# Kernel optimization log

Measured on AMD Instinct MI355X. Metric: run time of the kernel, lower is better.

The kernel has to match this reference:

```python
import jax, jax.numpy as jnp
import numpy as np

N, E, B, H, L = 100000, 200000, 2048, 256, 4
EPS_MSG = 1e-7   # GENConv message eps
LN_EPS = 1e-5    # torch LayerNorm default eps
SM_EPS = 1e-16   # PyG softmax denominator eps


def layer_norm(x, g, b):
    mu = x.mean(-1, keepdims=True)
    var = ((x - mu) ** 2).mean(-1, keepdims=True)
    return (x - mu) * jax.lax.rsqrt(var + LN_EPS) * g + b


def gen_conv(x, src, dst, eattr, t, W1, b1, lg, lb, W2, b2):
    # GENConv(aggr='softmax', learn_t, num_layers=2, norm='layer')
    msg = jax.nn.relu(x[src] + eattr) + EPS_MSG                      # [E,H]
    scaled = msg * t
    seg_max = jax.ops.segment_max(scaled, dst, num_segments=N)       # [N,H]
    seg_max = jnp.where(jnp.isfinite(seg_max), seg_max, 0.0)
    ex = jnp.exp(scaled - seg_max[dst])                              # [E,H]
    denom = jax.ops.segment_sum(ex, dst, num_segments=N)             # [N,H]
    alpha = ex / (denom[dst] + SM_EPS)
    out = jax.ops.segment_sum(msg * alpha, dst, num_segments=N)      # [N,H]
    out = out + x                                                    # root residual inside GENConv
    h = jax.nn.relu(layer_norm(out @ W1 + b1, lg, lb))               # MLP: Lin -> LN -> ReLU -> Lin
    return h @ W2 + b2


def setup_inputs() -> dict:
    key = jax.random.key(0)
    ks = iter(jax.random.split(key, 16))
    s = lambda *sh: jax.random.normal(next(ks), sh, jnp.float32) * 0.05
    return dict(
        x=jax.random.normal(next(ks), (N, 9), jnp.float32),
        edge_index=jax.random.randint(next(ks), (2, E), 0, N),
        edge_attr=jax.random.normal(next(ks), (E, 3), jnp.float32),
        batch=jnp.sort(jax.random.randint(next(ks), (N,), 0, B)),
        node_W=s(9, H), node_b=jnp.zeros((H,), jnp.float32),
        edge_W=s(3, H), edge_b=jnp.zeros((H,), jnp.float32),
        vn_emb=jnp.zeros((1, H), jnp.float32),
        ln_g=jnp.ones((L, H), jnp.float32), ln_b=jnp.zeros((L, H), jnp.float32),
        t=jnp.ones((L - 1,), jnp.float32),
        mlp_W1=s(L - 1, H, 2 * H), mlp_b1=jnp.zeros((L - 1, 2 * H), jnp.float32),
        mlp_ln_g=jnp.ones((L - 1, 2 * H), jnp.float32), mlp_ln_b=jnp.zeros((L - 1, 2 * H), jnp.float32),
        mlp_W2=s(L - 1, 2 * H, H), mlp_b2=jnp.zeros((L - 1, H), jnp.float32),
    )


def reference(x, edge_index, edge_attr, batch, node_W, node_b, edge_W, edge_b,
              vn_emb, ln_g, ln_b, t, mlp_W1, mlp_b1, mlp_ln_g, mlp_ln_b, mlp_W2, mlp_b2):
    src, dst = edge_index[0], edge_index[1]
    h = x @ node_W + node_b                                          # node encoder
    ea = edge_attr @ edge_W + edge_b                                 # edge encoder
    vn = jnp.broadcast_to(vn_emb, (B, H))
    counts = jax.ops.segment_sum(jnp.ones((N,), h.dtype), batch, num_segments=B)
    inv_counts = (1.0 / jnp.maximum(counts, 1.0))[:, None]           # [B,1]
    # layers[1:] run conv (block='res+'); layers[0] supplies only the final norm+act
    for l in range(1, L):
        hn = jax.nn.relu(layer_norm(h, ln_g[l], ln_b[l]))            # dropout=0.1 is a no-op in eval
        h = h + gen_conv(hn, src, dst, ea, t[l - 1],
                         mlp_W1[l - 1], mlp_b1[l - 1], mlp_ln_g[l - 1], mlp_ln_b[l - 1],
                         mlp_W2[l - 1], mlp_b2[l - 1])
        vn = vn + jax.ops.segment_sum(h, batch, num_segments=B) * inv_counts  # scatter_mean
        h = h + vn[batch]                                            # broadcast virtual node
    h = jax.nn.relu(layer_norm(h, ln_g[0], ln_b[0]))
    return jax.ops.segment_sum(h, batch, num_segments=B) * inv_counts  # global_mean_pool [B,H]
```

## Files before the change

kernel.cpp:

```cpp
#include <hip/hip_runtime.h>
#include <cstdint>
#include <cstddef>


typedef _Float16 half8_t __attribute__((ext_vector_type(8)));
typedef _Float16 half4_t __attribute__((ext_vector_type(4)));
typedef float    floatx4 __attribute__((ext_vector_type(4)));

#define DEVINL __device__ __forceinline__

DEVINL float wave_sum(float v) {
#pragma unroll
  for (int m = 32; m; m >>= 1) v += __shfl_xor(v, m, 64);
  return v;
}

__global__ __launch_bounds__(256) void k_node_enc(
    const float* __restrict__ x, const float* __restrict__ W,
    const float* __restrict__ bias, _Float16* __restrict__ h, int Nr) {
  __shared__ float sW[9 * 256];
  __shared__ float sb[256];
  __shared__ float sx[72];
  const int j = threadIdx.x;
#pragma unroll
  for (int k = 0; k < 9; ++k) sW[k * 256 + j] = W[k * 256 + j];
  sb[j] = bias[j];
  const int row0 = blockIdx.x * 8;
  if (j < 72) {
    int p = row0 * 9 + j;
    sx[j] = (p < Nr * 9) ? x[p] : 0.f;
  }
  __syncthreads();
  for (int r = 0; r < 8; ++r) {
    int row = row0 + r;
    if (row >= Nr) break;
    float acc = sb[j];
#pragma unroll
    for (int k = 0; k < 9; ++k) acc = fmaf(sx[r * 9 + k], sW[k * 256 + j], acc);
    h[(size_t)row * 256 + j] = (_Float16)acc;
  }
}

__global__ void k_bptr(const int* __restrict__ batch, int* __restrict__ bptr,
                       int N_, int B_) {
  int b = blockIdx.x * 256 + threadIdx.x;
  if (b > B_) return;
  int lo = 0, hi = N_;
  while (lo < hi) {
    int mid = (lo + hi) >> 1;
    if (batch[mid] < b) lo = mid + 1; else hi = mid;
  }
  bptr[b] = lo;
}

__global__ void k_deg(const int* __restrict__ ei, int* __restrict__ deg, int E_) {
  int e = blockIdx.x * 256 + threadIdx.x;
  if (e < E_) atomicAdd(&deg[ei[E_ + e]], 1);
}

__global__ __launch_bounds__(256) void k_scan1(
    const int* __restrict__ in, int* __restrict__ out1, int* __restrict__ bsum, int n) {
  __shared__ int tmp[256];
  const int t = threadIdx.x;
  const int base = blockIdx.x * 1024;
  int v[4];
  int run = 0;
#pragma unroll
  for (int i = 0; i < 4; ++i) {
    int p = base + t * 4 + i;
    int xv = (p < n) ? in[p] : 0;
    run += xv;
    v[i] = run;
  }
  tmp[t] = run;
  __syncthreads();
  for (int off = 1; off < 256; off <<= 1) {
    int u = (t >= off) ? tmp[t - off] : 0;
    __syncthreads();
    tmp[t] += u;
    __syncthreads();
  }
  int excl = tmp[t] - run;
#pragma unroll
  for (int i = 0; i < 4; ++i) {
    int p = base + t * 4 + i;
    if (p < n) out1[p] = v[i] + excl;
  }
  if (t == 255) bsum[blockIdx.x] = tmp[255];
}

__global__ void k_scan2(int* bsum, int nb, int* ptr0) {
  if (threadIdx.x == 0 && blockIdx.x == 0) {
    int run = 0;
    for (int i = 0; i < nb; ++i) { int xv = bsum[i]; bsum[i] = run; run += xv; }
    ptr0[0] = 0;
  }
}

__global__ __launch_bounds__(256) void k_scan3(
    int* out1, const int* __restrict__ bsum, int* __restrict__ cursor, int n) {
  int add = bsum[blockIdx.x];
  int p0 = blockIdx.x * 1024 + threadIdx.x * 4;
#pragma unroll
  for (int i = 0; i < 4; ++i) {
    int p = p0 + i;
    if (p < n) {
      int v = out1[p] + add;
      out1[p] = v;
      cursor[p + 1] = v;
    }
  }
  if (blockIdx.x == 0 && threadIdx.x == 0) cursor[0] = 0;
}

__global__ void k_csrfill(const int* __restrict__ ei, int* __restrict__ cursor,
                          int* __restrict__ csr_src, int* __restrict__ csr_eid, int E_) {
  int e = blockIdx.x * 256 + threadIdx.x;
  if (e < E_) {
    int d = ei[E_ + e];
    int pos = atomicAdd(&cursor[d], 1);
    csr_src[pos] = ei[e];
    csr_eid[pos] = e;
  }
}

__global__ void k_vninit(const float* __restrict__ emb, float* __restrict__ vn) {
  vn[(size_t)blockIdx.x * 256 + threadIdx.x] = emb[threadIdx.x];
}

__global__ __launch_bounds__(256) void k_wcvt_all(
    const float* __restrict__ W1, const float* __restrict__ W2,
    _Float16* __restrict__ W1T, _Float16* __restrict__ W2T) {
  int idx = blockIdx.x * 256 + threadIdx.x;
  int mat = idx >> 17;
  int rem = idx & 131071;
  if (mat < 3) {
    int k = rem >> 9, n = rem & 511;
    W1T[(size_t)mat * 131072 + (size_t)n * 256 + k] =
        (_Float16)W1[(size_t)mat * 131072 + rem];
  } else {
    int m = mat - 3;
    int k = rem >> 8, n = rem & 255;
    W2T[(size_t)m * 131072 + (size_t)n * 512 + k] =
        (_Float16)W2[(size_t)m * 131072 + rem];
  }
}

__global__ __launch_bounds__(256) void k_ln256(
    const _Float16* __restrict__ h, const float* __restrict__ g,
    const float* __restrict__ b, _Float16* __restrict__ out, int Nr) {
  int row = blockIdx.x * 4 + (threadIdx.x >> 6);
  if (row >= Nr) return;
  int lane = threadIdx.x & 63;
  half4_t xh = *(const half4_t*)(h + (size_t)row * 256 + lane * 4);
  float x0 = (float)xh[0], x1 = (float)xh[1], x2 = (float)xh[2], x3 = (float)xh[3];
  float s = wave_sum(x0 + x1 + x2 + x3);
  float mu = s * (1.f / 256.f);
  float d0 = x0 - mu, d1 = x1 - mu, d2 = x2 - mu, d3 = x3 - mu;
  float v = wave_sum(d0 * d0 + d1 * d1 + d2 * d2 + d3 * d3);
  float rstd = rsqrtf(v * (1.f / 256.f) + 1e-5f);
  float4 gv = *(const float4*)(g + lane * 4);
  float4 bv = *(const float4*)(b + lane * 4);
  half4_t o;
  o[0] = (_Float16)fmaxf(d0 * rstd * gv.x + bv.x, 0.f);
  o[1] = (_Float16)fmaxf(d1 * rstd * gv.y + bv.y, 0.f);
  o[2] = (_Float16)fmaxf(d2 * rstd * gv.z + bv.z, 0.f);
  o[3] = (_Float16)fmaxf(d3 * rstd * gv.w + bv.w, 0.f);
  *(half4_t*)(out + (size_t)row * 256 + lane * 4) = o;
}

__global__ __launch_bounds__(256) void k_aggregate(
    const _Float16* __restrict__ hn, const float* __restrict__ eattr,
    const float* __restrict__ edgeW, const float* __restrict__ edgeB,
    const int* __restrict__ indptr, const int* __restrict__ csr_src,
    const int* __restrict__ csr_eid, const float* __restrict__ tptr,
    _Float16* __restrict__ agg, int Nr) {
  int node = blockIdx.x * 4 + (threadIdx.x >> 6);
  if (node >= Nr) return;
  int lane = threadIdx.x & 63;
  int j0 = lane * 4;
  float4 w0 = *(const float4*)(edgeW + j0);
  float4 w1 = *(const float4*)(edgeW + 256 + j0);
  float4 w2 = *(const float4*)(edgeW + 512 + j0);
  float4 wb = *(const float4*)(edgeB + j0);
  float W0[4] = {w0.x, w0.y, w0.z, w0.w};
  float W1r[4] = {w1.x, w1.y, w1.z, w1.w};
  float W2r[4] = {w2.x, w2.y, w2.z, w2.w};
  float WB[4] = {wb.x, wb.y, wb.z, wb.w};
  float tval = tptr[0];
  int e0 = indptr[node], e1 = indptr[node + 1];
  float D[4] = {0.f, 0.f, 0.f, 0.f};
  float Nu[4] = {0.f, 0.f, 0.f, 0.f};
  for (int s = e0; s < e1; ++s) {
    int srcn = csr_src[s];
    int eid = csr_eid[s];
    float ex0 = eattr[(size_t)eid * 3 + 0];
    float ex1 = eattr[(size_t)eid * 3 + 1];
    float ex2 = eattr[(size_t)eid * 3 + 2];
    half4_t hv = *(const half4_t*)(hn + (size_t)srcn * 256 + j0);
#pragma unroll
    for (int i = 0; i < 4; ++i) {
      float eaj = fmaf(ex0, W0[i], fmaf(ex1, W1r[i], fmaf(ex2, W2r[i], WB[i])));
      float msg = fmaxf((float)hv[i] + eaj, 0.f) + 1e-7f;
      float pr = __expf(msg * tval);
      D[i] += pr;
      Nu[i] = fmaf(pr, msg, Nu[i]);
    }
  }
  half4_t hs = *(const half4_t*)(hn + (size_t)node * 256 + j0);
  half4_t res;
#pragma unroll
  for (int i = 0; i < 4; ++i)
    res[i] = (_Float16)(Nu[i] / (D[i] + 1e-16f) + (float)hs[i]);
  *(half4_t*)(agg + (size_t)node * 256 + j0) = res;
}

__global__ __launch_bounds__(256, 2) void k_gemm1(
    const _Float16* __restrict__ A, const _Float16* __restrict__ BT,
    const float* __restrict__ bias, _Float16* __restrict__ outh,
    float2* __restrict__ rstat, int M) {
  constexpr int EPS = 132;
  __shared__ _Float16 ldsA[64 * 256];
  __shared__ _Float16 ldsB[128 * 64];
  __shared__ _Float16 ldsE[4 * 16 * EPS];
  const int tid = threadIdx.x;
  const int lane = tid & 63;
  const int wv = tid >> 6;
  const int m0 = blockIdx.x * 64;
  const int wm = wv * 16;
  const int q = lane >> 4;
  const int l16 = lane & 15;
  _Float16* epi = ldsE + wv * (16 * EPS);

  {
    half8_t tmp[8];
    int ss[8];
#pragma unroll
    for (int g = 0; g < 8; ++g) {
      int s = g * 256 + tid;
      int r = s >> 5;
      int c = (s & 31) ^ (r & 7);
      int rowA = m0 + r;
      rowA = rowA < M ? rowA : (M - 1);
      tmp[g] = *(const half8_t*)(A + (size_t)rowA * 256 + c * 8);
      ss[g] = s;
    }
#pragma unroll
    for (int g = 0; g < 8; ++g)
      *(half8_t*)(ldsA + (size_t)ss[g] * 8) = tmp[g];
  }

  size_t offB[4];
  int ldsOffB[4];
#pragma unroll
  for (int i = 0; i < 4; ++i) {
    int p = (i * 4 + wv) * 64 + lane;
    int r = p >> 3;
    int s = p & 7;
    int gg = s ^ (r & 7);
    offB[i] = (size_t)r * 256 + gg * 8;
    ldsOffB[i] = p * 8;
  }
  half8_t rb[4];
  auto loadB = [&](int j) {
    int n = j >> 2, t = j & 3;
    size_t base = (size_t)n * 128 * 256 + t * 64;
#pragma unroll
    for (int i = 0; i < 4; ++i)
      rb[i] = *(const half8_t*)(BT + base + offB[i]);
  };
  auto writeB = [&]() {
#pragma unroll
    for (int i = 0; i < 4; ++i)
      *(half8_t*)(ldsB + ldsOffB[i]) = rb[i];
  };

  floatx4 acc[8] = {};
  float sA[4] = {0.f, 0.f, 0.f, 0.f}, s2A[4] = {0.f, 0.f, 0.f, 0.f};

  loadB(0);
  writeB();
  for (int j = 0; j < 16; ++j) {
    __syncthreads();
    if (j + 1 < 16) loadB(j + 1);
    const int t = j & 3;
#pragma unroll
    for (int kk = 0; kk < 2; ++kk) {
      const int c8 = kk * 4 + q;
      const int cg = t * 8 + c8;
      int r = wm + l16;
      half8_t af = *(const half8_t*)(ldsA + (size_t)(r * 32 + (cg ^ (r & 7))) * 8);
      half8_t bf[8];
#pragma unroll
      for (int ct = 0; ct < 8; ++ct) {
        int n = ct * 16 + l16;
        bf[ct] = *(const half8_t*)(ldsB + (size_t)(n * 8 + (c8 ^ (n & 7))) * 8);
      }
#pragma unroll
      for (int ct = 0; ct < 8; ++ct)
        acc[ct] = __builtin_amdgcn_mfma_f32_16x16x32_f16(af, bf[ct], acc[ct], 0, 0, 0);
    }
    __syncthreads();
    if (j + 1 < 16) writeB();
    if ((j & 3) == 3) {
      int n = j >> 2;
#pragma unroll
      for (int rr = 0; rr < 4; ++rr) {
        int rloc = q * 4 + rr;
        float s = 0.f, s2 = 0.f;
#pragma unroll
        for (int ct = 0; ct < 8; ++ct) {
          int col = n * 128 + ct * 16 + l16;
          float v = acc[ct][rr] + bias[col];
          epi[rloc * EPS + ct * 16 + l16] = (_Float16)v;
          s += v;
          s2 += v * v;
        }
        sA[rr] += s;
        s2A[rr] += s2;
      }
#pragma unroll
      for (int it = 0; it < 4; ++it) {
        int rloc = it * 4 + q;
        int row = m0 + wm + rloc;
        if (row < M) {
          half8_t ev = *(const half8_t*)(epi + rloc * EPS + l16 * 8);
          *(half8_t*)(outh + (size_t)row * 512 + n * 128 + l16 * 8) = ev;
        }
      }
#pragma unroll
      for (int ct = 0; ct < 8; ++ct)
        acc[ct] = floatx4{0.f, 0.f, 0.f, 0.f};
    }
  }

#pragma unroll
  for (int rr = 0; rr < 4; ++rr) {
    float s = sA[rr], s2 = s2A[rr];
#pragma unroll
    for (int m = 1; m < 16; m <<= 1) {
      s += __shfl_xor(s, m, 64);
      s2 += __shfl_xor(s2, m, 64);
    }
    int row = m0 + wm + q * 4 + rr;
    if (l16 == 0 && row < M) rstat[row] = make_float2(s, s2);
  }
}

template <int VN>
__global__ __launch_bounds__(256, 2) void k_gemm2(
    const _Float16* __restrict__ A, const _Float16* __restrict__ BT,
    const float* __restrict__ bias, const float2* __restrict__ rstat,
    const float* __restrict__ lg, const float* __restrict__ lb,
    const float* __restrict__ vn, const int* __restrict__ batch,
    _Float16* __restrict__ outf, int M) {
  constexpr int K = 512, NN = 256, NT = K / 64;
  constexpr int EPS = 68;
  const int g = blockIdx.x;
  const int mI = blockIdx.y * 8 + (g & 7);
  const int nI = g >> 3;
  const int mT = (M + 127) >> 7;
  if (mI >= mT) return;

  __shared__ _Float16 ldsbuf[4 * 64 * EPS];
  _Float16* ldsA = ldsbuf;
  _Float16* ldsB = ldsbuf + 128 * 64;
  __shared__ float sg[512];
  __shared__ float sbt[512];
  const int tid = threadIdx.x;
  sg[tid] = lg[tid];
  sg[tid + 256] = lg[tid + 256];
  sbt[tid] = lb[tid];
  sbt[tid + 256] = lb[tid + 256];
  __syncthreads();

  const int lane = tid & 63;
  const int wv = tid >> 6;
  const int m0 = mI * 128;
  const int n0 = nI * 128;
  const int wm = (wv >> 1) * 64;
  const int wn = (wv & 1) * 64;
  const int q = lane >> 4;
  const int l16 = lane & 15;
  floatx4 acc[4][4] = {};

  size_t offA[4], offB[4];
  int ldsOff[4], gcolA[4];
  float aco[4], cco[4];
#pragma unroll
  for (int i = 0; i < 4; ++i) {
    int p = (i * 4 + wv) * 64 + lane;
    int r = p >> 3;
    int s = p & 7;
    int gg = s ^ (r & 7);
    int rowA = m0 + r;
    rowA = rowA < M ? rowA : (M - 1);
    offA[i] = (size_t)rowA * K + gg * 8;
    offB[i] = (size_t)(n0 + r) * K + gg * 8;
    ldsOff[i] = p * 8;
    gcolA[i] = gg * 8;
    float2 st = rstat[rowA];
    float mu = st.x * (1.f / 512.f);
    float var = st.y * (1.f / 512.f) - mu * mu;
    float rs = rsqrtf(var + 1e-5f);
    aco[i] = rs;
    cco[i] = -mu * rs;
  }
  half8_t ra[4], rb[4];
  auto loadtile = [&](int kt) {
#pragma unroll
    for (int i = 0; i < 4; ++i) {
      ra[i] = *(const half8_t*)(A + offA[i] + kt);
      rb[i] = *(const half8_t*)(BT + offB[i] + kt);
    }
  };
  auto writetile = [&](int kt) {
#pragma unroll
    for (int i = 0; i < 4; ++i) {
      int c0 = kt + gcolA[i];
      half8_t ya;
#pragma unroll
      for (int jj = 0; jj < 8; ++jj) {
        float e = fmaf((float)ra[i][jj], aco[i], cco[i]);
        float y = fmaf(e, sg[c0 + jj], sbt[c0 + jj]);
        ya[jj] = (_Float16)fmaxf(y, 0.f);
      }
      *(half8_t*)(ldsA + ldsOff[i]) = ya;
      *(half8_t*)(ldsB + ldsOff[i]) = rb[i];
    }
  };

  loadtile(0);
  writetile(0);
#pragma unroll
  for (int t = 0; t < NT; ++t) {
    __syncthreads();
    if (t + 1 < NT) loadtile((t + 1) * 64);
#pragma unroll
    for (int kk = 0; kk < 2; ++kk) {
      half8_t af[4], bf[4];
      const int c8 = kk * 4 + q;
#pragma unroll
      for (int rt = 0; rt < 4; ++rt) {
        int r = wm + rt * 16 + l16;
        af[rt] = *(const half8_t*)(ldsA + (size_t)(r * 8 + (c8 ^ (r & 7))) * 8);
      }
#pragma unroll
      for (int ct = 0; ct < 4; ++ct) {
        int n = wn + ct * 16 + l16;
        bf[ct] = *(const half8_t*)(ldsB + (size_t)(n * 8 + (c8 ^ (n & 7))) * 8);
      }
#pragma unroll
      for (int rt = 0; rt < 4; ++rt)
#pragma unroll
        for (int ct = 0; ct < 4; ++ct)
          acc[rt][ct] = __builtin_amdgcn_mfma_f32_16x16x32_f16(af[rt], bf[ct], acc[rt][ct], 0, 0, 0);
    }
    __syncthreads();
    if (t + 1 < NT) writetile((t + 1) * 64);
  }

  _Float16* epi = ldsbuf + wv * (64 * EPS);
#pragma unroll
  for (int rt = 0; rt < 4; ++rt) {
#pragma unroll
    for (int rr = 0; rr < 4; ++rr) {
      int rloc = rt * 16 + q * 4 + rr;
      int row = m0 + wm + rloc;
      int rowc = row < M ? row : (M - 1);
      int bb = 0;
      if constexpr (VN) bb = batch[rowc];
#pragma unroll
      for (int ct = 0; ct < 4; ++ct) {
        int cloc = ct * 16 + l16;
        int col = n0 + wn + cloc;
        float v = acc[rt][ct][rr] + bias[col];
        if constexpr (VN) v += vn[(size_t)bb * 256 + col];
        epi[rloc * EPS + cloc] = (_Float16)v;
      }
    }
  }
#pragma unroll
  for (int it = 0; it < 8; ++it) {
    int rloc = it * 8 + (lane >> 3);
    int row = m0 + wm + rloc;
    if (row < M) {
      int c0 = (lane & 7) * 8;
      size_t gidx = (size_t)row * NN + n0 + wn + c0;
      half8_t hv = *(const half8_t*)(outf + gidx);
      half8_t ev = *(const half8_t*)(epi + rloc * EPS + c0);
      half8_t o;
#pragma unroll
      for (int jj = 0; jj < 8; ++jj) o[jj] = (_Float16)((float)hv[jj] + (float)ev[jj]);
      *(half8_t*)(outf + gidx) = o;
    }
  }
}

__global__ __launch_bounds__(256) void k_vnln(
    const _Float16* __restrict__ h, float* __restrict__ vn,
    const int* __restrict__ bptr, const float* __restrict__ g,
    const float* __restrict__ b, _Float16* __restrict__ hn) {
  __shared__ float red[3][256];
  __shared__ float svn[256];
  int bb = blockIdx.x;
  int w = threadIdx.x >> 6;
  int lane = threadIdx.x & 63;
  int n0 = bptr[bb], n1 = bptr[bb + 1];
  float a0 = 0.f, a1 = 0.f, a2 = 0.f, a3 = 0.f;
  for (int row = n0 + w; row < n1; row += 4) {
    half4_t xh = *(const half4_t*)(h + (size_t)row * 256 + lane * 4);
    a0 += (float)xh[0]; a1 += (float)xh[1];
    a2 += (float)xh[2]; a3 += (float)xh[3];
  }
  if (w > 0) {
    red[w - 1][lane * 4 + 0] = a0;
    red[w - 1][lane * 4 + 1] = a1;
    red[w - 1][lane * 4 + 2] = a2;
    red[w - 1][lane * 4 + 3] = a3;
  }
  __syncthreads();
  if (w == 0) {
    int c = n1 - n0;
    float ic = 1.f / (float)(c > 1 ? c : 1);
#pragma unroll
    for (int k = 0; k < 3; ++k) {
      a0 += red[k][lane * 4 + 0];
      a1 += red[k][lane * 4 + 1];
      a2 += red[k][lane * 4 + 2];
      a3 += red[k][lane * 4 + 3];
    }
    float4 vo = *(const float4*)(vn + (size_t)bb * 256 + lane * 4);
    vo.x += a0 * ic; vo.y += a1 * ic; vo.z += a2 * ic; vo.w += a3 * ic;
    *(float4*)(vn + (size_t)bb * 256 + lane * 4) = vo;
    svn[lane * 4 + 0] = vo.x;
    svn[lane * 4 + 1] = vo.y;
    svn[lane * 4 + 2] = vo.z;
    svn[lane * 4 + 3] = vo.w;
  }
  __syncthreads();
  float4 vv = *(const float4*)(svn + lane * 4);
  float4 gv = *(const float4*)(g + lane * 4);
  float4 bv = *(const float4*)(b + lane * 4);
  for (int row = n0 + w; row < n1; row += 4) {
    half4_t xh = *(const half4_t*)(h + (size_t)row * 256 + lane * 4);
    float x0 = (float)xh[0] + vv.x, x1 = (float)xh[1] + vv.y;
    float x2 = (float)xh[2] + vv.z, x3 = (float)xh[3] + vv.w;
    float s = wave_sum(x0 + x1 + x2 + x3);
    float mu = s * (1.f / 256.f);
    float d0 = x0 - mu, d1 = x1 - mu, d2 = x2 - mu, d3 = x3 - mu;
    float v = wave_sum(d0 * d0 + d1 * d1 + d2 * d2 + d3 * d3);
    float rstd = rsqrtf(v * (1.f / 256.f) + 1e-5f);
    half4_t o;
    o[0] = (_Float16)fmaxf(d0 * rstd * gv.x + bv.x, 0.f);
    o[1] = (_Float16)fmaxf(d1 * rstd * gv.y + bv.y, 0.f);
    o[2] = (_Float16)fmaxf(d2 * rstd * gv.z + bv.z, 0.f);
    o[3] = (_Float16)fmaxf(d3 * rstd * gv.w + bv.w, 0.f);
    *(half4_t*)(hn + (size_t)row * 256 + lane * 4) = o;
  }
}

__global__ __launch_bounds__(256) void k_vnlnpool(
    const _Float16* __restrict__ h, const float* __restrict__ vn,
    const int* __restrict__ bptr, const float* __restrict__ g,
    const float* __restrict__ b, float* __restrict__ out) {
  __shared__ float red[3][256];
  __shared__ float svn[256];
  int bb = blockIdx.x;
  int w = threadIdx.x >> 6;
  int lane = threadIdx.x & 63;
  int n0 = bptr[bb], n1 = bptr[bb + 1];
  int c = n1 - n0;
  float ic = 1.f / (float)(c > 1 ? c : 1);
  float a0 = 0.f, a1 = 0.f, a2 = 0.f, a3 = 0.f;
  for (int row = n0 + w; row < n1; row += 4) {
    half4_t xh = *(const half4_t*)(h + (size_t)row * 256 + lane * 4);
    a0 += (float)xh[0]; a1 += (float)xh[1];
    a2 += (float)xh[2]; a3 += (float)xh[3];
  }
  if (w > 0) {
    red[w - 1][lane * 4 + 0] = a0;
    red[w - 1][lane * 4 + 1] = a1;
    red[w - 1][lane * 4 + 2] = a2;
    red[w - 1][lane * 4 + 3] = a3;
  }
  __syncthreads();
  if (w == 0) {
#pragma unroll
    for (int k = 0; k < 3; ++k) {
      a0 += red[k][lane * 4 + 0];
      a1 += red[k][lane * 4 + 1];
      a2 += red[k][lane * 4 + 2];
      a3 += red[k][lane * 4 + 3];
    }
    float4 vo = *(const float4*)(vn + (size_t)bb * 256 + lane * 4);
    svn[lane * 4 + 0] = vo.x + a0 * ic;
    svn[lane * 4 + 1] = vo.y + a1 * ic;
    svn[lane * 4 + 2] = vo.z + a2 * ic;
    svn[lane * 4 + 3] = vo.w + a3 * ic;
  }
  __syncthreads();
  float4 vv = *(const float4*)(svn + lane * 4);
  float4 gv = *(const float4*)(g + lane * 4);
  float4 bv = *(const float4*)(b + lane * 4);
  a0 = a1 = a2 = a3 = 0.f;
  for (int row = n0 + w; row < n1; row += 4) {
    half4_t xh = *(const half4_t*)(h + (size_t)row * 256 + lane * 4);
    float x0 = (float)xh[0] + vv.x, x1 = (float)xh[1] + vv.y;
    float x2 = (float)xh[2] + vv.z, x3 = (float)xh[3] + vv.w;
    float s = wave_sum(x0 + x1 + x2 + x3);
    float mu = s * (1.f / 256.f);
    float d0 = x0 - mu, d1 = x1 - mu, d2 = x2 - mu, d3 = x3 - mu;
    float v = wave_sum(d0 * d0 + d1 * d1 + d2 * d2 + d3 * d3);
    float rstd = rsqrtf(v * (1.f / 256.f) + 1e-5f);
    a0 += fmaxf(d0 * rstd * gv.x + bv.x, 0.f);
    a1 += fmaxf(d1 * rstd * gv.y + bv.y, 0.f);
    a2 += fmaxf(d2 * rstd * gv.z + bv.z, 0.f);
    a3 += fmaxf(d3 * rstd * gv.w + bv.w, 0.f);
  }
  __syncthreads();
  if (w > 0) {
    red[w - 1][lane * 4 + 0] = a0;
    red[w - 1][lane * 4 + 1] = a1;
    red[w - 1][lane * 4 + 2] = a2;
    red[w - 1][lane * 4 + 3] = a3;
  }
  __syncthreads();
  if (w == 0) {
#pragma unroll
    for (int k = 0; k < 3; ++k) {
      a0 += red[k][lane * 4 + 0];
      a1 += red[k][lane * 4 + 1];
      a2 += red[k][lane * 4 + 2];
      a3 += red[k][lane * 4 + 3];
    }
    float4 o = {a0 * ic, a1 * ic, a2 * ic, a3 * ic};
    *(float4*)(out + (size_t)bb * 256 + lane * 4) = o;
  }
}

extern "C" void kernel_launch(void* const* d_in, const int* in_sizes, int n_in,
                              void* d_out, int out_size, void* d_ws, size_t ws_size,
                              hipStream_t stream) {
  const float* x      = (const float*)d_in[0];
  const int*   ei     = (const int*)d_in[1];
  const float* eattr  = (const float*)d_in[2];
  const int*   batch  = (const int*)d_in[3];
  const float* nodeW  = (const float*)d_in[4];
  const float* nodeB  = (const float*)d_in[5];
  const float* edgeW  = (const float*)d_in[6];
  const float* edgeB  = (const float*)d_in[7];
  const float* vnemb  = (const float*)d_in[8];
  const float* lng    = (const float*)d_in[9];
  const float* lnb    = (const float*)d_in[10];
  const float* tparam = (const float*)d_in[11];
  const float* W1     = (const float*)d_in[12];
  const float* b1     = (const float*)d_in[13];
  const float* mlng   = (const float*)d_in[14];
  const float* mlnb   = (const float*)d_in[15];
  const float* W2     = (const float*)d_in[16];
  const float* b2     = (const float*)d_in[17];
  float* out = (float*)d_out;

  const int N = in_sizes[3];
  const int E = in_sizes[1] / 2;
  const int B = out_size / 256;

  char* p = (char*)d_ws;
  auto take = [&](size_t bytes) -> char* {
    char* r = p;
    p += (bytes + 255) & ~(size_t)255;
    return r;
  };
  _Float16*  h   = (_Float16*)take((size_t)N * 256 * 2);
  _Float16*  t1  = (_Float16*)take((size_t)N * 512 * 2);
  _Float16*  hn  = t1;
  _Float16*  agg = (_Float16*)take((size_t)N * 256 * 2);
  _Float16*  W1T = (_Float16*)take((size_t)3 * 512 * 256 * 2);
  _Float16*  W2T = (_Float16*)take((size_t)3 * 256 * 512 * 2);
  float2*    rstat = (float2*)take((size_t)N * 8);
  float*     vn  = (float*)take((size_t)B * 256 * 4);
  int*       bptr   = (int*)take((size_t)(B + 1) * 4);
  int*       deg    = (int*)take((size_t)N * 4);
  int*       indptr = (int*)take((size_t)(N + 1) * 4);
  int*       cursor = (int*)take((size_t)(N + 1) * 4);
  int*       csr_src = (int*)take((size_t)E * 4);
  int*       csr_eid = (int*)take((size_t)E * 4);
  int*       bsum    = (int*)take(512 * 4);
  (void)ws_size; (void)n_in;

  hipMemsetAsync(deg, 0, (size_t)N * 4, stream);

  k_node_enc<<<(N + 7) / 8, 256, 0, stream>>>(x, nodeW, nodeB, h, N);
  k_bptr<<<(B + 256) / 256, 256, 0, stream>>>(batch, bptr, N, B);

  const int nbN = (N + 1023) / 1024;
  k_deg<<<(E + 255) / 256, 256, 0, stream>>>(ei, deg, E);
  k_scan1<<<nbN, 256, 0, stream>>>(deg, indptr + 1, bsum, N);
  k_scan2<<<1, 64, 0, stream>>>(bsum, nbN, indptr);
  k_scan3<<<nbN, 256, 0, stream>>>(indptr + 1, bsum, cursor, N);
  k_csrfill<<<(E + 255) / 256, 256, 0, stream>>>(ei, cursor, csr_src, csr_eid, E);

  k_wcvt_all<<<3072, 256, 0, stream>>>(W1, W2, W1T, W2T);
  k_vninit<<<B, 256, 0, stream>>>(vnemb, vn);

  const int lnGrid = (N + 3) / 4;
  const int mTiles1 = (N + 63) / 64;
  const int mTiles2 = (N + 127) / 128;
  const dim3 g2grid(16, (mTiles2 + 7) / 8);

  k_ln256<<<lnGrid, 256, 0, stream>>>(h, lng + 256, lnb + 256, hn, N);
  for (int l = 1; l <= 3; ++l) {
    k_aggregate<<<lnGrid, 256, 0, stream>>>(hn, eattr, edgeW, edgeB, indptr, csr_src, csr_eid,
                                            tparam + (l - 1), agg, N);
    k_gemm1<<<mTiles1, 256, 0, stream>>>(
        agg, W1T + (size_t)(l - 1) * 512 * 256, b1 + (size_t)(l - 1) * 512, t1, rstat, N);
    if (l == 1)
      k_gemm2<0><<<g2grid, 256, 0, stream>>>(
          t1, W2T + (size_t)(l - 1) * 256 * 512, b2 + (size_t)(l - 1) * 256, rstat,
          mlng + (size_t)(l - 1) * 512, mlnb + (size_t)(l - 1) * 512, nullptr, nullptr, h, N);
    else
      k_gemm2<1><<<g2grid, 256, 0, stream>>>(
          t1, W2T + (size_t)(l - 1) * 256 * 512, b2 + (size_t)(l - 1) * 256, rstat,
          mlng + (size_t)(l - 1) * 512, mlnb + (size_t)(l - 1) * 512, vn, batch, h, N);
    if (l < 3)
      k_vnln<<<B, 256, 0, stream>>>(h, vn, bptr,
                                    lng + (size_t)(l + 1) * 256, lnb + (size_t)(l + 1) * 256, hn);
    else
      k_vnlnpool<<<B, 256, 0, stream>>>(h, vn, bptr, lng, lnb, out);
  }
}
```

Measured before the change: 823.7 us.

## Double-buffer LDS tiles in both GEMMs and store gemm1 epilogue directly

Both GEMM kernels now keep two LDS tile buffers and alternate between them each k-step, so the second __syncthreads per iteration is dropped. The next tile is written into the other buffer while other waves may still be reading the current one. gemm1 also drops its LDS epilogue staging and writes scalar fp16 values straight to global memory, which frees LDS but turns 16-byte vector stores into 2-byte scattered stores. gemm2 gains a barrier after the loop so the epilogue can safely reuse the buffer.

```diff
diff --git a/kernel.cpp b/kernel.cpp
--- a/kernel.cpp
+++ b/kernel.cpp
@@ -219,10 +219,8 @@
     const _Float16* __restrict__ A, const _Float16* __restrict__ BT,
     const float* __restrict__ bias, _Float16* __restrict__ outh,
     float2* __restrict__ rstat, int M) {
-  constexpr int EPS = 132;
   __shared__ _Float16 ldsA[64 * 256];
-  __shared__ _Float16 ldsB[128 * 64];
-  __shared__ _Float16 ldsE[4 * 16 * EPS];
+  __shared__ _Float16 ldsB[2][128 * 64];
   const int tid = threadIdx.x;
   const int lane = tid & 63;
   const int wv = tid >> 6;
@@ -230,7 +228,6 @@
   const int wm = wv * 16;
   const int q = lane >> 4;
   const int l16 = lane & 15;
-  _Float16* epi = ldsE + wv * (16 * EPS);
 
   {
     half8_t tmp[8];
@@ -269,21 +266,22 @@
     for (int i = 0; i < 4; ++i)
       rb[i] = *(const half8_t*)(BT + base + offB[i]);
   };
-  auto writeB = [&]() {
+  auto writeB = [&](int buf) {
 #pragma unroll
     for (int i = 0; i < 4; ++i)
-      *(half8_t*)(ldsB + ldsOffB[i]) = rb[i];
+      *(half8_t*)(ldsB[buf] + ldsOffB[i]) = rb[i];
   };
 
   floatx4 acc[8] = {};
   float sA[4] = {0.f, 0.f, 0.f, 0.f}, s2A[4] = {0.f, 0.f, 0.f, 0.f};
 
   loadB(0);
-  writeB();
+  writeB(0);
   for (int j = 0; j < 16; ++j) {
     __syncthreads();
     if (j + 1 < 16) loadB(j + 1);
     const int t = j & 3;
+    const _Float16* Bc = ldsB[j & 1];
 #pragma unroll
     for (int kk = 0; kk < 2; ++kk) {
       const int c8 = kk * 4 + q;
@@ -294,39 +292,37 @@
 #pragma unroll
       for (int ct = 0; ct < 8; ++ct) {
         int n = ct * 16 + l16;
-        bf[ct] = *(const half8_t*)(ldsB + (size_t)(n * 8 + (c8 ^ (n & 7))) * 8);
+        bf[ct] = *(const half8_t*)(Bc + (size_t)(n * 8 + (c8 ^ (n & 7))) * 8);
       }
 #pragma unroll
       for (int ct = 0; ct < 8; ++ct)
         acc[ct] = __builtin_amdgcn_mfma_f32_16x16x32_f16(af, bf[ct], acc[ct], 0, 0, 0);
     }
-    __syncthreads();
-    if (j + 1 < 16) writeB();
+    if (j + 1 < 16) writeB((j + 1) & 1);
     if ((j & 3) == 3) {
       int n = j >> 2;
 #pragma unroll
       for (int rr = 0; rr < 4; ++rr) {
-        int rloc = q * 4 + rr;
+        int row = m0 + wm + q * 4 + rr;
+        float vv[8];
         float s = 0.f, s2 = 0.f;
 #pragma unroll
         for (int ct = 0; ct < 8; ++ct) {
           int col = n * 128 + ct * 16 + l16;
           float v = acc[ct][rr] + bias[col];
-          epi[rloc * EPS + ct * 16 + l16] = (_Float16)v;
+          vv[ct] = v;
           s += v;
           s2 += v * v;
         }
+        if (row < M) {
+#pragma unroll
+          for (int ct = 0; ct < 8; ++ct) {
+            int col = n * 128 + ct * 16 + l16;
+            outh[(size_t)row * 512 + col] = (_Float16)vv[ct];
+          }
+        }
         sA[rr] += s;
         s2A[rr] += s2;
-      }
-#pragma unroll
-      for (int it = 0; it < 4; ++it) {
-        int rloc = it * 4 + q;
-        int row = m0 + wm + rloc;
-        if (row < M) {
-          half8_t ev = *(const half8_t*)(epi + rloc * EPS + l16 * 8);
-          *(half8_t*)(outh + (size_t)row * 512 + n * 128 + l16 * 8) = ev;
-        }
       }
 #pragma unroll
       for (int ct = 0; ct < 8; ++ct)
@@ -362,9 +358,7 @@
   const int mT = (M + 127) >> 7;
   if (mI >= mT) return;
 
-  __shared__ _Float16 ldsbuf[4 * 64 * EPS];
-  _Float16* ldsA = ldsbuf;
-  _Float16* ldsB = ldsbuf + 128 * 64;
+  __shared__ _Float16 ldsbuf[32768];
   __shared__ float sg[512];
   __shared__ float sbt[512];
   const int tid = threadIdx.x;
@@ -414,7 +408,9 @@
       rb[i] = *(const half8_t*)(BT + offB[i] + kt);
     }
   };
-  auto writetile = [&](int kt) {
+  auto writetile = [&](int kt, int bsel) {
+    _Float16* dA = ldsbuf + bsel * 16384;
+    _Float16* dB = dA + 8192;
 #pragma unroll
     for (int i = 0; i < 4; ++i) {
       int c0 = kt + gcolA[i];
@@ -425,17 +421,19 @@
         float y = fmaf(e, sg[c0 + jj], sbt[c0 + jj]);
         ya[jj] = (_Float16)fmaxf(y, 0.f);
       }
-      *(half8_t*)(ldsA + ldsOff[i]) = ya;
-      *(half8_t*)(ldsB + ldsOff[i]) = rb[i];
+      *(half8_t*)(dA + ldsOff[i]) = ya;
+      *(half8_t*)(dB + ldsOff[i]) = rb[i];
     }
   };
 
   loadtile(0);
-  writetile(0);
+  writetile(0, 0);
 #pragma unroll
   for (int t = 0; t < NT; ++t) {
     __syncthreads();
     if (t + 1 < NT) loadtile((t + 1) * 64);
+    const _Float16* cA = ldsbuf + (t & 1) * 16384;
+    const _Float16* cB = cA + 8192;
 #pragma unroll
     for (int kk = 0; kk < 2; ++kk) {
       half8_t af[4], bf[4];
@@ -443,12 +441,12 @@
 #pragma unroll
       for (int rt = 0; rt < 4; ++rt) {
         int r = wm + rt * 16 + l16;
-        af[rt] = *(const half8_t*)(ldsA + (size_t)(r * 8 + (c8 ^ (r & 7))) * 8);
+        af[rt] = *(const half8_t*)(cA + (size_t)(r * 8 + (c8 ^ (r & 7))) * 8);
       }
 #pragma unroll
       for (int ct = 0; ct < 4; ++ct) {
         int n = wn + ct * 16 + l16;
-        bf[ct] = *(const half8_t*)(ldsB + (size_t)(n * 8 + (c8 ^ (n & 7))) * 8);
+        bf[ct] = *(const half8_t*)(cB + (size_t)(n * 8 + (c8 ^ (n & 7))) * 8);
       }
 #pragma unroll
       for (int rt = 0; rt < 4; ++rt)
@@ -456,9 +454,9 @@
         for (int ct = 0; ct < 4; ++ct)
           acc[rt][ct] = __builtin_amdgcn_mfma_f32_16x16x32_f16(af[rt], bf[ct], acc[rt][ct], 0, 0, 0);
     }
-    __syncthreads();
-    if (t + 1 < NT) writetile((t + 1) * 64);
-  }
+    if (t + 1 < NT) writetile((t + 1) * 64, (t + 1) & 1);
+  }
+  __syncthreads();
 
   _Float16* epi = ldsbuf + wv * (64 * EPS);
 #pragma unroll
```

After: 817.8 us. About the same (-0.7%).

## Fuse softmax edge aggregation into first MLP GEMM prologue

Applied to the files above, without the earlier changes.

Merges the per-node softmax aggregation kernel into the first GEMM. Each wave computes the aggregated rows for its 16 nodes and writes them straight into the swizzled LDS A tile, so the intermediate agg buffer is never written to or read back from global memory. The epilogue also drops its LDS staging buffer and stores fp16 results directly to global memory, and occupancy is raised to 3 blocks per CU. The cost is that the gather-bound aggregation now runs serially per wave before the MFMA loop, with far fewer waves in flight to hide gather latency, and the direct epilogue stores are scattered 2-byte writes instead of 16-byte vectors.

```diff
diff --git a/kernel.cpp b/kernel.cpp
--- a/kernel.cpp
+++ b/kernel.cpp
@@ -169,60 +169,15 @@
   *(half4_t*)(out + (size_t)row * 256 + lane * 4) = o;
 }
 
-__global__ __launch_bounds__(256) void k_aggregate(
+__global__ __launch_bounds__(256, 3) void k_agg_gemm1(
     const _Float16* __restrict__ hn, const float* __restrict__ eattr,
     const float* __restrict__ edgeW, const float* __restrict__ edgeB,
     const int* __restrict__ indptr, const int* __restrict__ csr_src,
     const int* __restrict__ csr_eid, const float* __restrict__ tptr,
-    _Float16* __restrict__ agg, int Nr) {
-  int node = blockIdx.x * 4 + (threadIdx.x >> 6);
-  if (node >= Nr) return;
-  int lane = threadIdx.x & 63;
-  int j0 = lane * 4;
-  float4 w0 = *(const float4*)(edgeW + j0);
-  float4 w1 = *(const float4*)(edgeW + 256 + j0);
-  float4 w2 = *(const float4*)(edgeW + 512 + j0);
-  float4 wb = *(const float4*)(edgeB + j0);
-  float W0[4] = {w0.x, w0.y, w0.z, w0.w};
-  float W1r[4] = {w1.x, w1.y, w1.z, w1.w};
-  float W2r[4] = {w2.x, w2.y, w2.z, w2.w};
-  float WB[4] = {wb.x, wb.y, wb.z, wb.w};
-  float tval = tptr[0];
-  int e0 = indptr[node], e1 = indptr[node + 1];
-  float D[4] = {0.f, 0.f, 0.f, 0.f};
-  float Nu[4] = {0.f, 0.f, 0.f, 0.f};
-  for (int s = e0; s < e1; ++s) {
-    int srcn = csr_src[s];
-    int eid = csr_eid[s];
-    float ex0 = eattr[(size_t)eid * 3 + 0];
-    float ex1 = eattr[(size_t)eid * 3 + 1];
-    float ex2 = eattr[(size_t)eid * 3 + 2];
-    half4_t hv = *(const half4_t*)(hn + (size_t)srcn * 256 + j0);
-#pragma unroll
-    for (int i = 0; i < 4; ++i) {
-      float eaj = fmaf(ex0, W0[i], fmaf(ex1, W1r[i], fmaf(ex2, W2r[i], WB[i])));
-      float msg = fmaxf((float)hv[i] + eaj, 0.f) + 1e-7f;
-      float pr = __expf(msg * tval);
-      D[i] += pr;
-      Nu[i] = fmaf(pr, msg, Nu[i]);
-    }
-  }
-  half4_t hs = *(const half4_t*)(hn + (size_t)node * 256 + j0);
-  half4_t res;
-#pragma unroll
-  for (int i = 0; i < 4; ++i)
-    res[i] = (_Float16)(Nu[i] / (D[i] + 1e-16f) + (float)hs[i]);
-  *(half4_t*)(agg + (size_t)node * 256 + j0) = res;
-}
-
-__global__ __launch_bounds__(256, 2) void k_gemm1(
-    const _Float16* __restrict__ A, const _Float16* __restrict__ BT,
-    const float* __restrict__ bias, _Float16* __restrict__ outh,
-    float2* __restrict__ rstat, int M) {
-  constexpr int EPS = 132;
+    const _Float16* __restrict__ BT, const float* __restrict__ bias,
+    _Float16* __restrict__ outh, float2* __restrict__ rstat, int M) {
   __shared__ _Float16 ldsA[64 * 256];
   __shared__ _Float16 ldsB[128 * 64];
-  __shared__ _Float16 ldsE[4 * 16 * EPS];
   const int tid = threadIdx.x;
   const int lane = tid & 63;
   const int wv = tid >> 6;
@@ -230,25 +185,6 @@
   const int wm = wv * 16;
   const int q = lane >> 4;
   const int l16 = lane & 15;
-  _Float16* epi = ldsE + wv * (16 * EPS);
-
-  {
-    half8_t tmp[8];
-    int ss[8];
-#pragma unroll
-    for (int g = 0; g < 8; ++g) {
-      int s = g * 256 + tid;
-      int r = s >> 5;
-      int c = (s & 31) ^ (r & 7);
-      int rowA = m0 + r;
-      rowA = rowA < M ? rowA : (M - 1);
-      tmp[g] = *(const half8_t*)(A + (size_t)rowA * 256 + c * 8);
-      ss[g] = s;
-    }
-#pragma unroll
-    for (int g = 0; g < 8; ++g)
-      *(half8_t*)(ldsA + (size_t)ss[g] * 8) = tmp[g];
-  }
 
   size_t offB[4];
   int ldsOffB[4];
@@ -274,12 +210,56 @@
     for (int i = 0; i < 4; ++i)
       *(half8_t*)(ldsB + ldsOffB[i]) = rb[i];
   };
+  loadB(0);
+
+  {
+    const int j0 = lane * 4;
+    float4 w0 = *(const float4*)(edgeW + j0);
+    float4 w1 = *(const float4*)(edgeW + 256 + j0);
+    float4 w2 = *(const float4*)(edgeW + 512 + j0);
+    float4 wb = *(const float4*)(edgeB + j0);
+    float W0[4] = {w0.x, w0.y, w0.z, w0.w};
+    float W1r[4] = {w1.x, w1.y, w1.z, w1.w};
+    float W2r[4] = {w2.x, w2.y, w2.z, w2.w};
+    float WB[4] = {wb.x, wb.y, wb.z, wb.w};
+    float tval = tptr[0];
+    for (int i = 0; i < 16; ++i) {
+      int r = wm + i;
+      int node = m0 + r;
+      half4_t res = {(_Float16)0.f, (_Float16)0.f, (_Float16)0.f, (_Float16)0.f};
+      if (node < M) {
+        int e0 = indptr[node], e1 = indptr[node + 1];
+        float D[4] = {0.f, 0.f, 0.f, 0.f};
+        float Nu[4] = {0.f, 0.f, 0.f, 0.f};
+        for (int s = e0; s < e1; ++s) {
+          int srcn = csr_src[s];
+          int eid = csr_eid[s];
+          float ex0 = eattr[(size_t)eid * 3 + 0];
+          float ex1 = eattr[(size_t)eid * 3 + 1];
+          float ex2 = eattr[(size_t)eid * 3 + 2];
+          half4_t hv = *(const half4_t*)(hn + (size_t)srcn * 256 + j0);
+#pragma unroll
+          for (int k = 0; k < 4; ++k) {
+            float eaj = fmaf(ex0, W0[k], fmaf(ex1, W1r[k], fmaf(ex2, W2r[k], WB[k])));
+            float msg = fmaxf((float)hv[k] + eaj, 0.f) + 1e-7f;
+            float pr = __expf(msg * tval);
+            D[k] += pr;
+            Nu[k] = fmaf(pr, msg, Nu[k]);
+          }
+        }
+        half4_t hs = *(const half4_t*)(hn + (size_t)node * 256 + j0);
+#pragma unroll
+        for (int k = 0; k < 4; ++k)
+          res[k] = (_Float16)(Nu[k] / (D[k] + 1e-16f) + (float)hs[k]);
+      }
+      int slot = r * 32 + ((lane >> 1) ^ (r & 7));
+      *(half4_t*)(ldsA + (size_t)slot * 8 + (lane & 1) * 4) = res;
+    }
+  }
+  writeB();
 
   floatx4 acc[8] = {};
   float sA[4] = {0.f, 0.f, 0.f, 0.f}, s2A[4] = {0.f, 0.f, 0.f, 0.f};
-
-  loadB(0);
-  writeB();
   for (int j = 0; j < 16; ++j) {
     __syncthreads();
     if (j + 1 < 16) loadB(j + 1);
@@ -306,27 +286,26 @@
       int n = j >> 2;
 #pragma unroll
       for (int rr = 0; rr < 4; ++rr) {
-        int rloc = q * 4 + rr;
+        int row = m0 + wm + q * 4 + rr;
+        float vv[8];
         float s = 0.f, s2 = 0.f;
 #pragma unroll
         for (int ct = 0; ct < 8; ++ct) {
           int col = n * 128 + ct * 16 + l16;
           float v = acc[ct][rr] + bias[col];
-          epi[rloc * EPS + ct * 16 + l16] = (_Float16)v;
+          vv[ct] = v;
           s += v;
           s2 += v * v;
         }
+        if (row < M) {
+#pragma unroll
+          for (int ct = 0; ct < 8; ++ct) {
+            int col = n * 128 + ct * 16 + l16;
+            outh[(size_t)row * 512 + col] = (_Float16)vv[ct];
+          }
+        }
         sA[rr] += s;
         s2A[rr] += s2;
-      }
-#pragma unroll
-      for (int it = 0; it < 4; ++it) {
-        int rloc = it * 4 + q;
-        int row = m0 + wm + rloc;
-        if (row < M) {
-          half8_t ev = *(const half8_t*)(epi + rloc * EPS + l16 * 8);
-          *(half8_t*)(outh + (size_t)row * 512 + n * 128 + l16 * 8) = ev;
-        }
       }
 #pragma unroll
       for (int ct = 0; ct < 8; ++ct)
@@ -674,8 +653,7 @@
   };
   _Float16*  h   = (_Float16*)take((size_t)N * 256 * 2);
   _Float16*  t1  = (_Float16*)take((size_t)N * 512 * 2);
-  _Float16*  hn  = t1;
-  _Float16*  agg = (_Float16*)take((size_t)N * 256 * 2);
+  _Float16*  hn  = (_Float16*)take((size_t)N * 256 * 2);
   _Float16*  W1T = (_Float16*)take((size_t)3 * 512 * 256 * 2);
   _Float16*  W2T = (_Float16*)take((size_t)3 * 256 * 512 * 2);
   float2*    rstat = (float2*)take((size_t)N * 8);
@@ -711,10 +689,9 @@
 
   k_ln256<<<lnGrid, 256, 0, stream>>>(h, lng + 256, lnb + 256, hn, N);
   for (int l = 1; l <= 3; ++l) {
-    k_aggregate<<<lnGrid, 256, 0, stream>>>(hn, eattr, edgeW, edgeB, indptr, csr_src, csr_eid,
-                                            tparam + (l - 1), agg, N);
-    k_gemm1<<<mTiles1, 256, 0, stream>>>(
-        agg, W1T + (size_t)(l - 1) * 512 * 256, b1 + (size_t)(l - 1) * 512, t1, rstat, N);
+    k_agg_gemm1<<<mTiles1, 256, 0, stream>>>(
+        hn, eattr, edgeW, edgeB, indptr, csr_src, csr_eid, tparam + (l - 1),
+        W1T + (size_t)(l - 1) * 512 * 256, b1 + (size_t)(l - 1) * 512, t1, rstat, N);
     if (l == 1)
       k_gemm2<0><<<g2grid, 256, 0, stream>>>(
           t1, W2T + (size_t)(l - 1) * 256 * 512, b2 + (size_t)(l - 1) * 256, rstat,
```

Result: slower. 878.8 us (+6.7%).
